# Optimization experiments

Measured on AMD Instinct MI355X. Metric: run time of the kernel, lower is better.

Reference implementation:

```python
import jax, jax.numpy as jnp
import numpy as np

B, S, D_IN, D_OUT = 4, 2048, 4096, 4096
SPARSE_FRACTION = 0.9


def setup_inputs() -> dict:
    key = jax.random.key(0)
    k_x, k_w, k_m = jax.random.split(key, 3)
    x = jax.random.normal(k_x, (B, S, D_IN), dtype=jnp.float32)
    # kaiming_uniform_(a=sqrt(5)) -> U(-bound, bound), bound = sqrt(6/((1+a^2)*fan_in)) = 1/sqrt(fan_in)
    bound = 1.0 / np.sqrt(D_IN)
    weight = jax.random.uniform(k_w, (D_OUT, D_IN), dtype=jnp.float32,
                                minval=-bound, maxval=bound)
    # mask: exactly (1 - sparse_fraction) of entries are True (random permutation)
    num_params = D_OUT * D_IN
    num_sparse = int(num_params * SPARSE_FRACTION)
    perm = jax.random.permutation(k_m, num_params)
    mask_flat = jnp.ones((num_params,), dtype=jnp.float32).at[perm[:num_sparse]].set(0.0)
    mask = mask_flat.reshape(D_OUT, D_IN).astype(jnp.bool_)
    return {"x": x, "weight": weight, "mask": mask}


def reference(x, weight, mask):
    # masked_weight = weight * mask; out = x @ masked_weight.T
    masked_weight = weight * mask.astype(weight.dtype)  # [out, in]
    return jnp.einsum('bsi,oi->bso', x, masked_weight)
```

## Files before the change

### kernel.cpp

```cpp
#include <hip/hip_runtime.h>
#include <stdint.h>


static constexpr int Mdim = 8192;
static constexpr int Ndim = 4096;
static constexpr int Kdim = 4096;
static constexpr int BM = 256;
static constexpr int BN = 256;
static constexpr int BK = 64;
static constexpr int NT = Kdim / BK;

typedef __attribute__((ext_vector_type(8))) short short8;
typedef __attribute__((ext_vector_type(4))) float float4v;
typedef __attribute__((ext_vector_type(4))) float f32x4;
typedef __attribute__((ext_vector_type(4))) int int4v;
typedef __attribute__((ext_vector_type(8))) unsigned short ushort8;

__device__ __forceinline__ unsigned short f32_to_bf16(float f) {
  union { float f; uint32_t u; } c; c.f = f;
  uint32_t u = c.u;
  u += 0x7fffu + ((u >> 16) & 1u);
  return (unsigned short)(u >> 16);
}

__global__ void detect_mask_kernel(const unsigned char* __restrict__ m, int* __restrict__ flag) {
  int found = 0;
  const int total = 1 << 20;
  for (int p = blockIdx.x * blockDim.x + threadIdx.x; p < total;
       p += gridDim.x * blockDim.x)
    found |= (m[4 * p + 1] != 0);
  if (__any(found) && (threadIdx.x & 63) == 0) atomicOr(flag, 1);
}

__global__ void cvt_x_kernel(const float* __restrict__ x, unsigned short* __restrict__ o) {
  long i = (blockIdx.x * (long)blockDim.x + threadIdx.x) * 8;
  float4v v0 = *(const float4v*)(x + i);
  float4v v1 = *(const float4v*)(x + i + 4);
  ushort8 r;
  r[0] = f32_to_bf16(v0[0]); r[1] = f32_to_bf16(v0[1]);
  r[2] = f32_to_bf16(v0[2]); r[3] = f32_to_bf16(v0[3]);
  r[4] = f32_to_bf16(v1[0]); r[5] = f32_to_bf16(v1[1]);
  r[6] = f32_to_bf16(v1[2]); r[7] = f32_to_bf16(v1[3]);
  *(ushort8*)(o + i) = r;
}

__global__ void cvt_w_kernel(const float* __restrict__ w, const unsigned char* __restrict__ mraw,
                             const int* __restrict__ flag, unsigned short* __restrict__ o) {
  long i = (blockIdx.x * (long)blockDim.x + threadIdx.x) * 8;
  float4v w0 = *(const float4v*)(w + i);
  float4v w1 = *(const float4v*)(w + i + 4);
  int m[8];
  if (*flag) {
    unsigned long long mb = *(const unsigned long long*)(mraw + i);
#pragma unroll
    for (int j = 0; j < 8; ++j) m[j] = ((mb >> (8 * j)) & 0xffull) != 0;
  } else {
    int4v a = *(const int4v*)((const int*)mraw + i);
    int4v b = *(const int4v*)((const int*)mraw + i + 4);
#pragma unroll
    for (int j = 0; j < 4; ++j) { m[j] = a[j] != 0; m[4 + j] = b[j] != 0; }
  }
  ushort8 r;
  r[0] = f32_to_bf16(m[0] ? w0[0] : 0.0f);
  r[1] = f32_to_bf16(m[1] ? w0[1] : 0.0f);
  r[2] = f32_to_bf16(m[2] ? w0[2] : 0.0f);
  r[3] = f32_to_bf16(m[3] ? w0[3] : 0.0f);
  r[4] = f32_to_bf16(m[4] ? w1[0] : 0.0f);
  r[5] = f32_to_bf16(m[5] ? w1[1] : 0.0f);
  r[6] = f32_to_bf16(m[6] ? w1[2] : 0.0f);
  r[7] = f32_to_bf16(m[7] ? w1[3] : 0.0f);
  *(ushort8*)(o + i) = r;
}


__device__ __forceinline__ void stage_half(const unsigned short* __restrict__ src,
                                           int grow_base, int kelem, char* region,
                                           int r0, int l0, int gcol) {
  const unsigned short* g0 = src + (size_t)(grow_base + r0) * Kdim + kelem + gcol;
  const unsigned short* g1 = src + (size_t)(grow_base + r0 + 8) * Kdim + kelem + gcol;
  __builtin_amdgcn_global_load_lds((const __attribute__((address_space(1))) void*)g0,
                                   (__attribute__((address_space(3))) void*)(region + l0),
                                   16, 0, 0);
  __builtin_amdgcn_global_load_lds((const __attribute__((address_space(1))) void*)g1,
                                   (__attribute__((address_space(3))) void*)(region + l0 + 1024),
                                   16, 0, 0);
}

template <int BUF, int MI0>
__device__ __forceinline__ void load_a(short8 (&a)[4][2], const char* sA,
                                       int wm, int arow, int kg, int w7) {
#pragma unroll
  for (int mi = 0; mi < 4; ++mi) {
    const char* rowp = sA + (BUF * 2 + wm) * 16384 + ((MI0 + mi) * 16 + arow) * 128;
#pragma unroll
    for (int s = 0; s < 2; ++s)
      a[mi][s] = *(const short8*)(rowp + (((s << 2) | kg) ^ w7) * 16);
  }
}

template <int BUF, int NI0>
__device__ __forceinline__ void load_b(short8 (&b)[4][2], const char* sB,
                                       int wnh, int brow, int kg, int w7) {
#pragma unroll
  for (int ni = 0; ni < 2; ++ni) {
    const char* rowp = sB + (BUF * 2 + wnh) * 16384 + (brow + (NI0 + ni) * 16) * 128;
#pragma unroll
    for (int s = 0; s < 2; ++s)
      b[NI0 + ni][s] = *(const short8*)(rowp + (((s << 2) | kg) ^ w7) * 16);
  }
}

template <int MIB, int NIB>
__device__ __forceinline__ void mfma_quad(f32x4 (&acc)[8][4], const short8 (&a)[4][2],
                                          const short8 (&b)[4][2]) {
#pragma unroll
  for (int s = 0; s < 2; ++s)
#pragma unroll
    for (int mi = 0; mi < 4; ++mi)
#pragma unroll
      for (int ni = 0; ni < 2; ++ni)
        acc[MIB + mi][NIB + ni] = __builtin_amdgcn_mfma_f32_16x16x32_bf16(
            a[mi][s], b[NIB + ni][s], acc[MIB + mi][NIB + ni], 0, 0, 0);
}

__device__ __forceinline__ void phase_pre() {
  __builtin_amdgcn_sched_barrier(0);
  __builtin_amdgcn_s_barrier();
  asm volatile("s_waitcnt lgkmcnt(0)" ::: "memory");
  __builtin_amdgcn_sched_barrier(0);
  __builtin_amdgcn_s_setprio(1);
}

__device__ __forceinline__ void phase_post() {
  __builtin_amdgcn_s_setprio(0);
  __builtin_amdgcn_sched_barrier(0);
  __builtin_amdgcn_s_barrier();
}

__device__ __forceinline__ void phase_post_vm() {
  __builtin_amdgcn_s_setprio(0);
  __builtin_amdgcn_sched_barrier(0);
  asm volatile("s_waitcnt vmcnt(4)" ::: "memory");
  __builtin_amdgcn_sched_barrier(0);
  __builtin_amdgcn_s_barrier();
}

__global__ __launch_bounds__(512, 2) void gemm_bt_kernel(const unsigned short* __restrict__ X,
                                                         const unsigned short* __restrict__ W,
                                                         float* __restrict__ O) {
  __shared__ __align__(16) char lds[131072];
  char* sA = lds;
  char* sB = lds + 65536;

  const int tid = threadIdx.x;
  const int lane = tid & 63;
  const int wave = tid >> 6;
  const int wm = wave >> 2;
  const int wn = wave & 3;
  const int wnh = wn >> 1;

  const int bid = blockIdx.x;
  const int id = (bid & 7) * 64 + (bid >> 3);
  const int tm = id >> 4;
  const int tn = id & 15;
  const int row0 = tm * BM;
  const int col0 = tn * BN;

  const int r0 = wave * 16 + (lane >> 3);
  const int gcol = ((lane & 7) ^ (lane >> 3)) * 8;
  const int l0 = wave * 2048 + lane * 16;

  const int arow = lane & 15;
  const int kg = lane >> 4;
  const int w7 = lane & 7;
  const int brow = (wn & 1) * 64 + arow;

  f32x4 acc[8][4];
#pragma unroll
  for (int i = 0; i < 8; ++i)
#pragma unroll
    for (int j = 0; j < 4; ++j)
#pragma unroll
      for (int r = 0; r < 4; ++r) acc[i][j][r] = 0.f;

  short8 a[4][2], b[4][2];

  stage_half(X, row0 + 0,   0 * BK, sA + 0 * 16384, r0, l0, gcol);
  stage_half(X, row0 + 128, 0 * BK, sA + 1 * 16384, r0, l0, gcol);
  stage_half(W, col0 + 0,   0 * BK, sB + 0 * 16384, r0, l0, gcol);
  stage_half(W, col0 + 128, 0 * BK, sB + 1 * 16384, r0, l0, gcol);
  stage_half(W, col0 + 0,   1 * BK, sB + 2 * 16384, r0, l0, gcol);
  stage_half(W, col0 + 128, 1 * BK, sB + 3 * 16384, r0, l0, gcol);
  asm volatile("s_waitcnt vmcnt(4)" ::: "memory");
  __builtin_amdgcn_sched_barrier(0);
  __builtin_amdgcn_s_barrier();

#pragma unroll 1
  for (int it = 0; it < NT / 2; ++it) {
    const int t1 = 2 * it + 1;
    const int t2 = (2 * it + 2) & (NT - 1);
    const int t3 = (2 * it + 3) & (NT - 1);

    load_a<0, 0>(a, sA, wm, arow, kg, w7);
    load_b<0, 0>(b, sB, wnh, brow, kg, w7);
    stage_half(X, row0 + 0, t1 * BK, sA + 2 * 16384, r0, l0, gcol);
    phase_pre(); mfma_quad<0, 0>(acc, a, b); phase_post();
    load_b<0, 2>(b, sB, wnh, brow, kg, w7);
    stage_half(X, row0 + 128, t1 * BK, sA + 3 * 16384, r0, l0, gcol);
    phase_pre(); mfma_quad<0, 2>(acc, a, b); phase_post();
    load_a<0, 4>(a, sA, wm, arow, kg, w7);
    stage_half(W, col0 + 0, t2 * BK, sB + 0 * 16384, r0, l0, gcol);
    phase_pre(); mfma_quad<4, 0>(acc, a, b); phase_post();
    stage_half(W, col0 + 128, t2 * BK, sB + 1 * 16384, r0, l0, gcol);
    phase_pre(); mfma_quad<4, 2>(acc, a, b); phase_post_vm();

    load_a<1, 0>(a, sA, wm, arow, kg, w7);
    load_b<1, 0>(b, sB, wnh, brow, kg, w7);
    stage_half(X, row0 + 0, t2 * BK, sA + 0 * 16384, r0, l0, gcol);
    phase_pre(); mfma_quad<0, 0>(acc, a, b); phase_post();
    load_b<1, 2>(b, sB, wnh, brow, kg, w7);
    stage_half(X, row0 + 128, t2 * BK, sA + 1 * 16384, r0, l0, gcol);
    phase_pre(); mfma_quad<0, 2>(acc, a, b); phase_post();
    load_a<1, 4>(a, sA, wm, arow, kg, w7);
    stage_half(W, col0 + 0, t3 * BK, sB + 2 * 16384, r0, l0, gcol);
    phase_pre(); mfma_quad<4, 0>(acc, a, b); phase_post();
    stage_half(W, col0 + 128, t3 * BK, sB + 3 * 16384, r0, l0, gcol);
    phase_pre(); mfma_quad<4, 2>(acc, a, b); phase_post_vm();
  }

  const int orow0 = row0 + wm * 128 + kg * 4;
  const int ocol0 = col0 + wn * 64 + arow;
#pragma unroll
  for (int mi = 0; mi < 8; ++mi)
#pragma unroll
    for (int ni = 0; ni < 4; ++ni)
#pragma unroll
      for (int r = 0; r < 4; ++r)
        O[(size_t)(orow0 + mi * 16 + r) * Ndim + ocol0 + ni * 16] = acc[mi][ni][r];
}

__global__ void gemm_fallback_kernel(const float* __restrict__ X, const float* __restrict__ Wt,
                                     const unsigned char* __restrict__ mraw,
                                     const int* __restrict__ flag, float* __restrict__ O) {
  __shared__ float sX[16][17];
  __shared__ float sW[16][17];
  const int tx = threadIdx.x & 15;
  const int ty = threadIdx.x >> 4;
  const long row = blockIdx.y * 16 + ty;
  const long colblock = blockIdx.x * 16;
  const int byteLayout = *flag;
  float acc = 0.f;
  for (int k0 = 0; k0 < Kdim; k0 += 16) {
    sX[ty][tx] = X[row * Kdim + k0 + tx];
    const long wi = (colblock + ty) * (long)Kdim + k0 + tx;
    const int mv = byteLayout ? (mraw[wi] != 0) : (((const int*)mraw)[wi] != 0);
    sW[ty][tx] = mv ? Wt[wi] : 0.f;
    __syncthreads();
#pragma unroll
    for (int k = 0; k < 16; ++k) acc += sX[ty][k] * sW[tx][k];
    __syncthreads();
  }
  O[row * Ndim + colblock + tx] = acc;
}

extern "C" void kernel_launch(void* const* d_in, const int* in_sizes, int n_in,
                              void* d_out, int out_size, void* d_ws, size_t ws_size,
                              hipStream_t stream) {
  const float* x = (const float*)d_in[0];
  const float* w = (const float*)d_in[1];
  const unsigned char* mask = (const unsigned char*)d_in[2];
  float* out = (float*)d_out;

  const size_t xb_off = 0;
  const size_t wb_off = (size_t)Mdim * Kdim * 2;
  const size_t flag_off = wb_off + (size_t)Ndim * Kdim * 2;
  const size_t needed = flag_off + 16;

  if (ws_size >= needed) {
    unsigned short* xb = (unsigned short*)((char*)d_ws + xb_off);
    unsigned short* wb = (unsigned short*)((char*)d_ws + wb_off);
    int* flag = (int*)((char*)d_ws + flag_off);

    hipMemsetAsync(flag, 0, sizeof(int), stream);
    detect_mask_kernel<<<64, 256, 0, stream>>>(mask, flag);
    cvt_x_kernel<<<(int)(((long)Mdim * Kdim / 8) / 256), 256, 0, stream>>>(x, xb);
    cvt_w_kernel<<<(int)(((long)Ndim * Kdim / 8) / 256), 256, 0, stream>>>(w, mask, flag, wb);
    gemm_bt_kernel<<<(Mdim / BM) * (Ndim / BN), 512, 0, stream>>>(xb, wb, out);
  } else {
    int* flag = (int*)d_ws;
    hipMemsetAsync(flag, 0, sizeof(int), stream);
    detect_mask_kernel<<<64, 256, 0, stream>>>(mask, flag);
    dim3 grid(Ndim / 16, Mdim / 16);
    gemm_fallback_kernel<<<grid, 256, 0, stream>>>(x, w, mask, flag, out);
  }
}
```

Measured before the change: 537.5 us.

## Triple-buffer A tiles in LDS to deepen prefetch and hoist global addresses

The kernel now keeps three rotating LDS buffers for the X tile instead of two, so X loads for a K-step are issued a full step earlier and the wait threshold rises from vmcnt(4) to vmcnt(8). Global source pointers are precomputed once and advanced by a K offset, which removes per-stage index arithmetic. LDS use grows from 128 KB to 160 KB per block. With __launch_bounds__(512,2), two blocks can no longer share one CU's LDS, so occupancy may drop to one block per CU.

```diff
diff --git a/kernel.cpp b/kernel.cpp
--- a/kernel.cpp
+++ b/kernel.cpp
@@ -73,37 +73,34 @@
 }
 
 
-__device__ __forceinline__ void stage_half(const unsigned short* __restrict__ src,
-                                           int grow_base, int kelem, char* region,
-                                           int r0, int l0, int gcol) {
-  const unsigned short* g0 = src + (size_t)(grow_base + r0) * Kdim + kelem + gcol;
-  const unsigned short* g1 = src + (size_t)(grow_base + r0 + 8) * Kdim + kelem + gcol;
-  __builtin_amdgcn_global_load_lds((const __attribute__((address_space(1))) void*)g0,
-                                   (__attribute__((address_space(3))) void*)(region + l0),
-                                   16, 0, 0);
-  __builtin_amdgcn_global_load_lds((const __attribute__((address_space(1))) void*)g1,
-                                   (__attribute__((address_space(3))) void*)(region + l0 + 1024),
-                                   16, 0, 0);
-}
-
-template <int BUF, int MI0>
-__device__ __forceinline__ void load_a(short8 (&a)[4][2], const char* sA,
-                                       int wm, int arow, int kg, int w7) {
+__device__ __forceinline__ void gload16(const unsigned short* g, char* l) {
+  __builtin_amdgcn_global_load_lds((const __attribute__((address_space(1))) void*)g,
+                                   (__attribute__((address_space(3))) void*)l, 16, 0, 0);
+}
+
+__device__ __forceinline__ void stage_half(const unsigned short* g0, char* region, int l0) {
+  gload16(g0, region + l0);
+  gload16(g0 + 8 * Kdim, region + l0 + 1024);
+}
+
+template <int MI0>
+__device__ __forceinline__ void load_a(short8 (&a)[4][2], const char* baseA,
+                                       int arow, int kg, int w7) {
 #pragma unroll
   for (int mi = 0; mi < 4; ++mi) {
-    const char* rowp = sA + (BUF * 2 + wm) * 16384 + ((MI0 + mi) * 16 + arow) * 128;
+    const char* rowp = baseA + ((MI0 + mi) * 16 + arow) * 128;
 #pragma unroll
     for (int s = 0; s < 2; ++s)
       a[mi][s] = *(const short8*)(rowp + (((s << 2) | kg) ^ w7) * 16);
   }
 }
 
-template <int BUF, int NI0>
-__device__ __forceinline__ void load_b(short8 (&b)[4][2], const char* sB,
-                                       int wnh, int brow, int kg, int w7) {
+template <int NI0>
+__device__ __forceinline__ void load_b(short8 (&b)[4][2], const char* baseB,
+                                       int brow, int kg, int w7) {
 #pragma unroll
   for (int ni = 0; ni < 2; ++ni) {
-    const char* rowp = sB + (BUF * 2 + wnh) * 16384 + (brow + (NI0 + ni) * 16) * 128;
+    const char* rowp = baseB + (brow + (NI0 + ni) * 16) * 128;
 #pragma unroll
     for (int s = 0; s < 2; ++s)
       b[NI0 + ni][s] = *(const short8*)(rowp + (((s << 2) | kg) ^ w7) * 16);
@@ -140,7 +137,7 @@
 __device__ __forceinline__ void phase_post_vm() {
   __builtin_amdgcn_s_setprio(0);
   __builtin_amdgcn_sched_barrier(0);
-  asm volatile("s_waitcnt vmcnt(4)" ::: "memory");
+  asm volatile("s_waitcnt vmcnt(8)" ::: "memory");
   __builtin_amdgcn_sched_barrier(0);
   __builtin_amdgcn_s_barrier();
 }
@@ -148,9 +145,9 @@
 __global__ __launch_bounds__(512, 2) void gemm_bt_kernel(const unsigned short* __restrict__ X,
                                                          const unsigned short* __restrict__ W,
                                                          float* __restrict__ O) {
-  __shared__ __align__(16) char lds[131072];
+  __shared__ __align__(16) char lds[163840];
   char* sA = lds;
-  char* sB = lds + 65536;
+  char* sB = lds + 98304;
 
   const int tid = threadIdx.x;
   const int lane = tid & 63;
@@ -170,11 +167,19 @@
   const int gcol = ((lane & 7) ^ (lane >> 3)) * 8;
   const int l0 = wave * 2048 + lane * 16;
 
+  const unsigned short* gA0 = X + (size_t)(row0 + r0) * Kdim + gcol;
+  const unsigned short* gA1 = gA0 + (size_t)128 * Kdim;
+  const unsigned short* gB0 = W + (size_t)(col0 + r0) * Kdim + gcol;
+  const unsigned short* gB1 = gB0 + (size_t)128 * Kdim;
+
   const int arow = lane & 15;
   const int kg = lane >> 4;
   const int w7 = lane & 7;
   const int brow = (wn & 1) * 64 + arow;
 
+  const char* pBe = sB + wnh * 16384;
+  const char* pBo = sB + 32768 + wnh * 16384;
+
   f32x4 acc[8][4];
 #pragma unroll
   for (int i = 0; i < 8; ++i)
@@ -185,47 +190,58 @@
 
   short8 a[4][2], b[4][2];
 
-  stage_half(X, row0 + 0,   0 * BK, sA + 0 * 16384, r0, l0, gcol);
-  stage_half(X, row0 + 128, 0 * BK, sA + 1 * 16384, r0, l0, gcol);
-  stage_half(W, col0 + 0,   0 * BK, sB + 0 * 16384, r0, l0, gcol);
-  stage_half(W, col0 + 128, 0 * BK, sB + 1 * 16384, r0, l0, gcol);
-  stage_half(W, col0 + 0,   1 * BK, sB + 2 * 16384, r0, l0, gcol);
-  stage_half(W, col0 + 128, 1 * BK, sB + 3 * 16384, r0, l0, gcol);
-  asm volatile("s_waitcnt vmcnt(4)" ::: "memory");
+  stage_half(gA0,      sA + 0,     l0);
+  stage_half(gA1,      sA + 16384, l0);
+  stage_half(gB0,      sB + 0,     l0);
+  stage_half(gB1,      sB + 16384, l0);
+  stage_half(gA0 + BK, sA + 32768, l0);
+  stage_half(gA1 + BK, sA + 49152, l0);
+  stage_half(gB0 + BK, sB + 32768, l0);
+  stage_half(gB1 + BK, sB + 49152, l0);
+  asm volatile("s_waitcnt vmcnt(8)" ::: "memory");
   __builtin_amdgcn_sched_barrier(0);
   __builtin_amdgcn_s_barrier();
 
+  int ra = 0;
 #pragma unroll 1
   for (int it = 0; it < NT / 2; ++it) {
-    const int t1 = 2 * it + 1;
-    const int t2 = (2 * it + 2) & (NT - 1);
-    const int t3 = (2 * it + 3) & (NT - 1);
-
-    load_a<0, 0>(a, sA, wm, arow, kg, w7);
-    load_b<0, 0>(b, sB, wnh, brow, kg, w7);
-    stage_half(X, row0 + 0, t1 * BK, sA + 2 * 16384, r0, l0, gcol);
+    const int rb = (ra == 2) ? 0 : ra + 1;
+    const int ba = (rb == 2) ? 0 : rb + 1;
+    const int bb = ra;
+    const int k2 = ((2 * it + 2) & (NT - 1)) * BK;
+    const int k3 = ((2 * it + 3) & (NT - 1)) * BK;
+    const char* pAr0 = sA + (ra * 2 + wm) * 16384;
+    const char* pAr1 = sA + (rb * 2 + wm) * 16384;
+    char* pAs0 = sA + ba * 32768;
+    char* pAs1 = sA + bb * 32768;
+
+    load_a<0>(a, pAr0, arow, kg, w7);
+    load_b<0>(b, pBe, brow, kg, w7);
+    stage_half(gA0 + k2, pAs0, l0);
     phase_pre(); mfma_quad<0, 0>(acc, a, b); phase_post();
-    load_b<0, 2>(b, sB, wnh, brow, kg, w7);
-    stage_half(X, row0 + 128, t1 * BK, sA + 3 * 16384, r0, l0, gcol);
+    load_b<2>(b, pBe, brow, kg, w7);
+    stage_half(gA1 + k2, pAs0 + 16384, l0);
     phase_pre(); mfma_quad<0, 2>(acc, a, b); phase_post();
-    load_a<0, 4>(a, sA, wm, arow, kg, w7);
-    stage_half(W, col0 + 0, t2 * BK, sB + 0 * 16384, r0, l0, gcol);
+    load_a<4>(a, pAr0, arow, kg, w7);
+    stage_half(gB0 + k2, sB + 0, l0);
     phase_pre(); mfma_quad<4, 0>(acc, a, b); phase_post();
-    stage_half(W, col0 + 128, t2 * BK, sB + 1 * 16384, r0, l0, gcol);
+    stage_half(gB1 + k2, sB + 16384, l0);
     phase_pre(); mfma_quad<4, 2>(acc, a, b); phase_post_vm();
 
-    load_a<1, 0>(a, sA, wm, arow, kg, w7);
-    load_b<1, 0>(b, sB, wnh, brow, kg, w7);
-    stage_half(X, row0 + 0, t2 * BK, sA + 0 * 16384, r0, l0, gcol);
+    load_a<0>(a, pAr1, arow, kg, w7);
+    load_b<0>(b, pBo, brow, kg, w7);
+    stage_half(gA0 + k3, pAs1, l0);
     phase_pre(); mfma_quad<0, 0>(acc, a, b); phase_post();
-    load_b<1, 2>(b, sB, wnh, brow, kg, w7);
-    stage_half(X, row0 + 128, t2 * BK, sA + 1 * 16384, r0, l0, gcol);
+    load_b<2>(b, pBo, brow, kg, w7);
+    stage_half(gA1 + k3, pAs1 + 16384, l0);
     phase_pre(); mfma_quad<0, 2>(acc, a, b); phase_post();
-    load_a<1, 4>(a, sA, wm, arow, kg, w7);
-    stage_half(W, col0 + 0, t3 * BK, sB + 2 * 16384, r0, l0, gcol);
+    load_a<4>(a, pAr1, arow, kg, w7);
+    stage_half(gB0 + k3, sB + 32768, l0);
     phase_pre(); mfma_quad<4, 0>(acc, a, b); phase_post();
-    stage_half(W, col0 + 128, t3 * BK, sB + 3 * 16384, r0, l0, gcol);
+    stage_half(gB1 + k3, sB + 49152, l0);
     phase_pre(); mfma_quad<4, 2>(acc, a, b); phase_post_vm();
+
+    ra = ba;
   }
 
   const int orow0 = row0 + wm * 128 + kg * 4;
```

After: 541.8 us. Within noise of the previous version (+0.8%).
